# Performance work log

Hardware: AMD Instinct MI355X
Metric: run time of the kernel (lower is better)

The kernel has to match this reference:

```python
import jax, jax.numpy as jnp
import numpy as np

H = 16  # attention heads


def setup_inputs() -> dict:
    key = jax.random.key(0)
    k0, k1, k2 = jax.random.split(key, 3)
    B, T, C = 2, 2048, 1024
    x = jax.random.normal(k0, (B, T, C), dtype=jnp.float32)
    W_attn = jax.random.normal(k1, (3 * C, C), dtype=jnp.float32) * 0.02
    W_proj = jax.random.normal(k2, (C, C), dtype=jnp.float32) * 0.02
    b_proj = jnp.zeros((C,), dtype=jnp.float32)
    return {"x": x, "W_attn": W_attn, "W_proj": W_proj, "b_proj": b_proj}


def reference(x, W_attn, W_proj, b_proj):
    # Eval-mode (dropout = identity), rotational_embeddings=False, flash=False path.
    B, T, C = x.shape
    d = C // H
    qkv = jnp.einsum('btc,fc->btf', x, W_attn)          # [B,T,3C] fused QKV proj
    q, k, v = jnp.split(qkv, 3, axis=-1)
    # [B,T,C] -> [B,H,T,d]
    q = q.reshape(B, T, H, d).transpose(0, 2, 1, 3)
    k = k.reshape(B, T, H, d).transpose(0, 2, 1, 3)
    v = v.reshape(B, T, H, d).transpose(0, 2, 1, 3)
    scale = 1.0 / np.sqrt(d).astype(np.float32)
    att = jnp.einsum('bhqd,bhkd->bhqk', q, k) * scale    # full TxT scores (no mask)
    att = jax.nn.softmax(att, axis=-1)
    y = jnp.einsum('bhqk,bhkd->bhqd', att, v)            # [B,H,T,d]
    y = y.transpose(0, 2, 1, 3).reshape(B, T, C)
    return jnp.einsum('btc,oc->bto', y, W_proj) + b_proj
```

## Files before the change

### kernel.cpp

```cpp
#include <hip/hip_runtime.h>
#include <hip/hip_bf16.h>
#include <stdint.h>

typedef __attribute__((ext_vector_type(8))) short bf16x8;
typedef __attribute__((ext_vector_type(4))) float f32x4;
typedef __attribute__((ext_vector_type(4))) unsigned u32x4;

#define MFMA16(A,B,C) __builtin_amdgcn_mfma_f32_16x16x32_bf16(A,B,C,0,0,0)


__device__ inline void gld_lds16(const __hip_bfloat16* g, __hip_bfloat16* l) {
  __builtin_amdgcn_global_load_lds(
      (const __attribute__((address_space(1))) void*)g,
      (__attribute__((address_space(3))) void*)l, 16, 0, 0);
}

__device__ inline unsigned pkbf(float a, float b) {
  __hip_bfloat162 t = __float22bfloat162_rn(float2{a, b});
  return *(unsigned*)&t;
}

__device__ inline void quad_mix(unsigned &a, unsigned &b) {
#if __has_builtin(__builtin_amdgcn_permlane32_swap) && __has_builtin(__builtin_amdgcn_permlane16_swap)
  auto r1 = __builtin_amdgcn_permlane32_swap(a, b, false, false);
  auto r2 = __builtin_amdgcn_permlane16_swap(r1[0], r1[1], false, false);
  a = r2[0];
  b = r2[1];
#else
  int lane = (int)(threadIdx.x & 63);
  int g = lane >> 4;
  int lm = lane & 15;
  int slo = (((g << 1) & 3) << 4) | lm;
  int shi = ((((g << 1) | 1) & 3) << 4) | lm;
  unsigned t0 = (unsigned)__shfl((int)a, slo, 64);
  unsigned t1 = (unsigned)__shfl((int)b, slo, 64);
  unsigned t2 = (unsigned)__shfl((int)a, shi, 64);
  unsigned t3 = (unsigned)__shfl((int)b, shi, 64);
  bool hi = g >= 2;
  unsigned na = hi ? t1 : t0;
  unsigned nb = hi ? t3 : t2;
  a = na;
  b = nb;
#endif
}

__global__ __launch_bounds__(256)
void cvt_bf16(const float* __restrict__ s0, __hip_bfloat16* __restrict__ d0, int n0,
              const float* __restrict__ s1, __hip_bfloat16* __restrict__ d1, int n1,
              const float* __restrict__ s2, __hip_bfloat16* __restrict__ d2, int n2)
{
  const float* s; __hip_bfloat16* d; int n;
  if      (blockIdx.y == 0) { s = s0; d = d0; n = n0; }
  else if (blockIdx.y == 1) { s = s1; d = d1; n = n1; }
  else                      { s = s2; d = d2; n = n2; }
  int idx = (blockIdx.x * 256 + threadIdx.x) * 8;
  if (idx >= n) return;
  float4 u0 = *(const float4*)(s + idx);
  float4 u1 = *(const float4*)(s + idx + 4);
  __hip_bfloat16 t[8];
  t[0] = __float2bfloat16(u0.x); t[1] = __float2bfloat16(u0.y);
  t[2] = __float2bfloat16(u0.z); t[3] = __float2bfloat16(u0.w);
  t[4] = __float2bfloat16(u1.x); t[5] = __float2bfloat16(u1.y);
  t[6] = __float2bfloat16(u1.z); t[7] = __float2bfloat16(u1.w);
  *(int4*)(d + idx) = *(const int4*)t;
}

template<int BM, int BN, typename TC>
__global__ __launch_bounds__(256)
void gemm_bt(const __hip_bfloat16* __restrict__ A,
             const __hip_bfloat16* __restrict__ B,
             TC* __restrict__ C,
             const float* __restrict__ bias,
             __hip_bfloat16* __restrict__ vtg,
             int M, int N, int K)
{
  constexpr int MI = BM / 32;
  constexpr int NJ = BN / 32;
  constexpr int NP = (BM + BN) / 64;

  __shared__ __align__(16) __hip_bfloat16 As[BM * 32];
  __shared__ __align__(16) __hip_bfloat16 Bs[BN * 32];

  const int tid  = threadIdx.x;
  const int lane = tid & 63;
  const int w    = tid >> 6;
  const int lm   = lane & 15;
  const int g    = lane >> 4;

  const int bm = blockIdx.y * BM;
  const int bn = blockIdx.x * BN;
  const int rm = (w >> 1) * (BM / 2);
  const int cn = (w & 1) * (BN / 2);

  const f32x4 fzero = {0.0f, 0.0f, 0.0f, 0.0f};
  f32x4 acc[MI][NJ];
  for (int i = 0; i < MI; i++)
    for (int j = 0; j < NJ; j++)
      acc[i][j] = fzero;

  for (int k0 = 0; k0 < K; k0 += 32) {
    __syncthreads();
#pragma unroll
    for (int p = 0; p < NP; p++) {
      int c = tid + p * 256;
      if (c < BM * 4)
        gld_lds16(&A[(size_t)(bm + (c >> 2)) * K + k0 + (c & 3) * 8], &As[c * 8]);
      else {
        int cb = c - BM * 4;
        gld_lds16(&B[(size_t)(bn + (cb >> 2)) * K + k0 + (cb & 3) * 8], &Bs[cb * 8]);
      }
    }
    __syncthreads();

    bf16x8 af[MI], bfr[NJ];
#pragma unroll
    for (int i = 0; i < MI; i++)
      af[i] = *(const bf16x8*)&As[(rm + 16 * i + lm) * 32 + 8 * g];
#pragma unroll
    for (int j = 0; j < NJ; j++)
      bfr[j] = *(const bf16x8*)&Bs[(cn + 16 * j + lm) * 32 + 8 * g];
#pragma unroll
    for (int i = 0; i < MI; i++)
#pragma unroll
      for (int j = 0; j < NJ; j++)
        acc[i][j] = MFMA16(af[i], bfr[j], acc[i][j]);
  }

  if (vtg != nullptr && bn >= 2048) {
#pragma unroll
    for (int j = 0; j < NJ; j++) {
      int colv = bn + cn + 16 * j + lm - 2048;
      int vh = colv >> 6, dd = colv & 63;
#pragma unroll
      for (int i = 0; i < MI; i++) {
        int m0 = bm + rm + 16 * i + 4 * g;
        int bb = m0 >> 11, t0 = m0 & 2047;
        __hip_bfloat16 t4[4];
#pragma unroll
        for (int r = 0; r < 4; r++) t4[r] = __float2bfloat16(acc[i][j][r]);
        *(int2*)&vtg[((size_t)(bb * 16 + vh) * 64 + dd) * 2048 + t0] =
            *(const int2*)t4;
      }
    }
    return;
  }

  const float qs = (vtg != nullptr && bn < 1024) ? (0.125f * 1.4426950408889634f)
                                                 : 1.0f;
#pragma unroll
  for (int j = 0; j < NJ; j++) {
    int coln = bn + cn + 16 * j + lm;
    float bv = bias ? bias[coln] : 0.0f;
#pragma unroll
    for (int i = 0; i < MI; i++) {
#pragma unroll
      for (int r = 0; r < 4; r++) {
        int rowm = bm + rm + 16 * i + 4 * g + r;
        float v = acc[i][j][r] * qs + bv;
        if constexpr (sizeof(TC) == 2)
          C[(size_t)rowm * N + coln] = __float2bfloat16(v);
        else
          C[(size_t)rowm * N + coln] = v;
      }
    }
  }
}

__global__ __launch_bounds__(256)
void mha(const __hip_bfloat16* __restrict__ qkv,
         const __hip_bfloat16* __restrict__ vtg,
         __hip_bfloat16* __restrict__ yout,
         __hip_bfloat16* __restrict__ po,
         float* __restrict__ pl,
         int nsteps)
{
  const int T = 2048, F = 3072, Cc = 1024;
  const int bh = blockIdx.x;
  const int b  = bh >> 4, h = bh & 15;
  const int qb0 = blockIdx.y * 128;
  const int z   = blockIdx.z;
  const int kvb = z * 32 * nsteps;

  const int tid  = threadIdx.x;
  const int lane = tid & 63;
  const int w    = tid >> 6;
  const int lm   = lane & 15;
  const int g    = lane >> 4;

  __shared__ __align__(16) __hip_bfloat16 Ks[2][32 * 64];
  __shared__ __align__(16) __hip_bfloat16 Vs[2][64 * 32];

  const size_t rowbase = (size_t)b * T * F;
  const int hoff = h * 64;
  const __hip_bfloat16* Kbase = qkv + rowbase + 1024 + hoff;
  const __hip_bfloat16* Vtb   = vtg + (size_t)(b * 16 + h) * 64 * 2048;

  const int qw = qb0 + 32 * w;
  bf16x8 aq[2][2];
#pragma unroll
  for (int mt = 0; mt < 2; mt++)
#pragma unroll
    for (int e = 0; e < 2; e++)
      aq[mt][e] = *(const bf16x8*)
          &qkv[rowbase + (size_t)(qw + 16 * mt + lm) * F + hoff + 32 * e + 8 * g];

  const f32x4 fzero = {0.0f, 0.0f, 0.0f, 0.0f};
  const short one_bf = (short)0x3f80;
  const bf16x8 vone = {one_bf, one_bf, one_bf, one_bf,
                       one_bf, one_bf, one_bf, one_bf};
  f32x4 yacc[2][4];
  f32x4 yl[2];
#pragma unroll
  for (int mt = 0; mt < 2; mt++) {
    yl[mt] = fzero;
#pragma unroll
    for (int c = 0; c < 4; c++) yacc[mt][c] = fzero;
  }

  const int r0  = tid >> 3;
  const int swK = (tid & 7) ^ (r0 & 7);
  const int vdd = tid >> 2;
  const int vk  = (tid & 3) ^ ((tid >> 3) & 3);
  const int sxK = lm & 7;
  const int sxV = (lm >> 1) & 3;

  gld_lds16(Kbase + (size_t)(kvb + r0) * F + swK * 8, &Ks[0][tid * 8]);
  gld_lds16(Vtb + (size_t)vdd * 2048 + kvb + vk * 8, &Vs[0][tid * 8]);

  for (int t = 0; t < nsteps; t++) {
    const int buf = t & 1;
    __syncthreads();
    if (t + 1 < nsteps) {
      const int kvn = kvb + (t + 1) * 32;
      gld_lds16(Kbase + (size_t)(kvn + r0) * F + swK * 8, &Ks[buf ^ 1][tid * 8]);
      gld_lds16(Vtb + (size_t)vdd * 2048 + kvn + vk * 8, &Vs[buf ^ 1][tid * 8]);
    }

    bf16x8 kf[2][2];
#pragma unroll
    for (int c2 = 0; c2 < 2; c2++) {
      kf[c2][0] = *(const bf16x8*)&Ks[buf][(16 * c2 + lm) * 64 + ((0 + g) ^ sxK) * 8];
      kf[c2][1] = *(const bf16x8*)&Ks[buf][(16 * c2 + lm) * 64 + ((4 + g) ^ sxK) * 8];
    }

    bf16x8 ap[2];
#pragma unroll
    for (int mt = 0; mt < 2; mt++) {
      f32x4 st[2];
      __builtin_amdgcn_s_setprio(1);
#pragma unroll
      for (int c2 = 0; c2 < 2; c2++) {
        st[c2] = MFMA16(kf[c2][0], aq[mt][0], fzero);
        st[c2] = MFMA16(kf[c2][1], aq[mt][1], st[c2]);
      }
      __builtin_amdgcn_s_setprio(0);

      unsigned pkv[2][2];
#pragma unroll
      for (int c2 = 0; c2 < 2; c2++)
#pragma unroll
        for (int u = 0; u < 2; u++) {
          float p0 = __builtin_amdgcn_exp2f(st[c2][2 * u]);
          float p1 = __builtin_amdgcn_exp2f(st[c2][2 * u + 1]);
          pkv[c2][u] = pkbf(p0, p1);
        }

      unsigned f0 = pkv[0][0], f2 = pkv[1][0];
      quad_mix(f0, f2);
      unsigned f1 = pkv[0][1], f3 = pkv[1][1];
      quad_mix(f1, f3);
      u32x4 fv = {f0, f1, f2, f3};
      ap[mt] = __builtin_bit_cast(bf16x8, fv);
    }

    __builtin_amdgcn_s_setprio(1);
#pragma unroll
    for (int c = 0; c < 4; c++) {
      bf16x8 bv = *(const bf16x8*)&Vs[buf][(16 * c + lm) * 32 + (g ^ sxV) * 8];
      yacc[0][c] = MFMA16(ap[0], bv, yacc[0][c]);
      yacc[1][c] = MFMA16(ap[1], bv, yacc[1][c]);
    }
    yl[0] = MFMA16(ap[0], vone, yl[0]);
    yl[1] = MFMA16(ap[1], vone, yl[1]);
    __builtin_amdgcn_s_setprio(0);
  }

#pragma unroll
  for (int mt = 0; mt < 2; mt++) {
    if (yout != nullptr) {
      float rv[4];
#pragma unroll
      for (int r = 0; r < 4; r++)
        rv[r] = 1.0f / yl[mt][r];
#pragma unroll
      for (int c = 0; c < 4; c++)
#pragma unroll
        for (int r = 0; r < 4; r++) {
          int qrow = qw + 16 * mt + 4 * g + r;
          yout[(size_t)(b * T + qrow) * Cc + hoff + 16 * c + lm] =
              __float2bfloat16(yacc[mt][c][r] * rv[r]);
        }
    } else {
      __hip_bfloat16* pz = po + (size_t)z * 4096 * 1024;
      float* plz = pl + (size_t)z * 4096 * 16;
#pragma unroll
      for (int c = 0; c < 4; c++)
#pragma unroll
        for (int r = 0; r < 4; r++) {
          int qrow = qw + 16 * mt + 4 * g + r;
          pz[(size_t)(b * T + qrow) * Cc + hoff + 16 * c + lm] =
              __float2bfloat16(yacc[mt][c][r]);
        }
      if (lm == 0) {
#pragma unroll
        for (int r = 0; r < 4; r++)
          plz[(b * T + qw + 16 * mt + 4 * g + r) * 16 + h] = yl[mt][r];
      }
    }
  }
}

template<int Z>
__global__ __launch_bounds__(256)
void combine(const __hip_bfloat16* __restrict__ po,
             const float* __restrict__ pl,
             __hip_bfloat16* __restrict__ y)
{
  int idx = (blockIdx.x * 256 + threadIdx.x) * 8;
  int row = idx >> 10, c = idx & 1023, h = c >> 6;
  float l = 0.0f;
#pragma unroll
  for (int zi = 0; zi < Z; zi++)
    l += pl[zi * 4096 * 16 + row * 16 + h];
  float rinv = 1.0f / l;
  float acc[8] = {0.f, 0.f, 0.f, 0.f, 0.f, 0.f, 0.f, 0.f};
#pragma unroll
  for (int zi = 0; zi < Z; zi++) {
    int4 raw = *(const int4*)(po + (size_t)zi * 4096 * 1024 + idx);
    const __hip_bfloat16* pa = (const __hip_bfloat16*)&raw;
#pragma unroll
    for (int j = 0; j < 8; j++) acc[j] += __bfloat162float(pa[j]);
  }
  __hip_bfloat16 t[8];
#pragma unroll
  for (int j = 0; j < 8; j++) t[j] = __float2bfloat16(acc[j] * rinv);
  *(int4*)(y + idx) = *(const int4*)t;
}

extern "C" void kernel_launch(void* const* d_in, const int* in_sizes, int n_in,
                              void* d_out, int out_size, void* d_ws, size_t ws_size,
                              hipStream_t stream)
{
  const float* x  = (const float*)d_in[0];
  const float* Wa = (const float*)d_in[1];
  const float* Wp = (const float*)d_in[2];
  const float* bp = (const float*)d_in[3];
  float* out = (float*)d_out;

  const int BT = 4096, C = 1024, F3 = 3072;
  char* ws = (char*)d_ws;
  __hip_bfloat16* qkv  = (__hip_bfloat16*)ws;
  __hip_bfloat16* vtg  = (__hip_bfloat16*)(ws + 25165824);
  __hip_bfloat16* xbf  = (__hip_bfloat16*)(ws + 33554432);
  __hip_bfloat16* yb   = xbf;
  __hip_bfloat16* Wabf = (__hip_bfloat16*)(ws + 41943040);
  __hip_bfloat16* Wpbf = (__hip_bfloat16*)(ws + 48234496);
  __hip_bfloat16* Opar = (__hip_bfloat16*)(ws + 50331648);
  float*          lpar = (float*)(ws + 67108864);
  const size_t need_split = 67633152;

  cvt_bf16<<<dim3(2048, 3), 256, 0, stream>>>(
      x, xbf, BT * C, Wa, Wabf, F3 * C, Wp, Wpbf, C * C);
  gemm_bt<128, 128, __hip_bfloat16>
      <<<dim3(F3 / 128, BT / 128), 256, 0, stream>>>(xbf, Wabf, qkv, nullptr, vtg,
                                                     BT, F3, C);
  if (ws_size >= need_split) {
    mha<<<dim3(32, 16, 2), 256, 0, stream>>>(qkv, vtg, nullptr, Opar, lpar, 32);
    combine<2><<<dim3(BT * C / 2048), 256, 0, stream>>>(Opar, lpar, yb);
  } else {
    mha<<<dim3(32, 16, 1), 256, 0, stream>>>(qkv, vtg, yb, nullptr, nullptr, 64);
  }
  gemm_bt<64, 128, float>
      <<<dim3(C / 128, BT / 64), 256, 0, stream>>>(yb, Wpbf, out, bp, nullptr,
                                                   BT, C, C);
}
```

Measured before the change: 207.0 us.

## Triple-buffer K/V LDS staging with explicit vmcnt waits in attention loop

Changes the attention kernel's K/V shared-memory staging from double to triple buffering, prefetching two tiles ahead. A manual s_waitcnt vmcnt plus a raw s_barrier replace __syncthreads, so loads for the following tile can stay in flight across the barrier. The intent is to hide more global-load latency per step. In exchange it uses 50% more LDS, which may reduce occupancy, and the hand-written waitcnt logic is fragile if the compiler issues other vector-memory ops.

After: 206.5 us. No clear change (-0.2%).

```diff
diff --git a/kernel.cpp b/kernel.cpp
--- a/kernel.cpp
+++ b/kernel.cpp
@@ -187,8 +187,8 @@
   const int lm   = lane & 15;
   const int g    = lane >> 4;
 
-  __shared__ __align__(16) __hip_bfloat16 Ks[2][32 * 64];
-  __shared__ __align__(16) __hip_bfloat16 Vs[2][64 * 32];
+  __shared__ __align__(16) __hip_bfloat16 Ks[3][32 * 64];
+  __shared__ __align__(16) __hip_bfloat16 Vs[3][64 * 32];
 
   const size_t rowbase = (size_t)b * T * F;
   const int hoff = h * 64;
@@ -224,23 +224,38 @@
   const int sxK = lm & 7;
   const int sxV = (lm >> 1) & 3;
 
-  gld_lds16(Kbase + (size_t)(kvb + r0) * F + swK * 8, &Ks[0][tid * 8]);
-  gld_lds16(Vtb + (size_t)vdd * 2048 + kvb + vk * 8, &Vs[0][tid * 8]);
-
+  auto stage = [&](int tt, int bb) {
+    const int kvn = kvb + tt * 32;
+    gld_lds16(Kbase + (size_t)(kvn + r0) * F + swK * 8, &Ks[bb][tid * 8]);
+    gld_lds16(Vtb + (size_t)vdd * 2048 + kvn + vk * 8, &Vs[bb][tid * 8]);
+  };
+
+  stage(0, 0);
+  if (nsteps > 1) stage(1, 1);
+
+  int bcur = 0;
   for (int t = 0; t < nsteps; t++) {
-    const int buf = t & 1;
-    __syncthreads();
-    if (t + 1 < nsteps) {
-      const int kvn = kvb + (t + 1) * 32;
-      gld_lds16(Kbase + (size_t)(kvn + r0) * F + swK * 8, &Ks[buf ^ 1][tid * 8]);
-      gld_lds16(Vtb + (size_t)vdd * 2048 + kvn + vk * 8, &Vs[buf ^ 1][tid * 8]);
-    }
+    if (t + 1 < nsteps)
+      asm volatile("s_waitcnt vmcnt(2)" ::: "memory");
+    else
+      asm volatile("s_waitcnt vmcnt(0)" ::: "memory");
+    __builtin_amdgcn_s_barrier();
+    __builtin_amdgcn_sched_barrier(0);
+
+    if (t + 2 < nsteps) {
+      int bnx = bcur + 2; if (bnx >= 3) bnx -= 3;
+      stage(t + 2, bnx);
+    }
+    __builtin_amdgcn_sched_barrier(0);
+
+    const __hip_bfloat16* Kb = Ks[bcur];
+    const __hip_bfloat16* Vb = Vs[bcur];
 
     bf16x8 kf[2][2];
 #pragma unroll
     for (int c2 = 0; c2 < 2; c2++) {
-      kf[c2][0] = *(const bf16x8*)&Ks[buf][(16 * c2 + lm) * 64 + ((0 + g) ^ sxK) * 8];
-      kf[c2][1] = *(const bf16x8*)&Ks[buf][(16 * c2 + lm) * 64 + ((4 + g) ^ sxK) * 8];
+      kf[c2][0] = *(const bf16x8*)&Kb[(16 * c2 + lm) * 64 + ((0 + g) ^ sxK) * 8];
+      kf[c2][1] = *(const bf16x8*)&Kb[(16 * c2 + lm) * 64 + ((4 + g) ^ sxK) * 8];
     }
 
     bf16x8 ap[2];
@@ -276,13 +291,15 @@
     __builtin_amdgcn_s_setprio(1);
 #pragma unroll
     for (int c = 0; c < 4; c++) {
-      bf16x8 bv = *(const bf16x8*)&Vs[buf][(16 * c + lm) * 32 + (g ^ sxV) * 8];
+      bf16x8 bv = *(const bf16x8*)&Vb[(16 * c + lm) * 32 + (g ^ sxV) * 8];
       yacc[0][c] = MFMA16(ap[0], bv, yacc[0][c]);
       yacc[1][c] = MFMA16(ap[1], bv, yacc[1][c]);
     }
     yl[0] = MFMA16(ap[0], vone, yl[0]);
     yl[1] = MFMA16(ap[1], vone, yl[1]);
     __builtin_amdgcn_s_setprio(0);
+
+    bcur = bcur + 1; if (bcur >= 3) bcur = 0;
   }
 
 #pragma unroll
```

## Double attention KV tile to 64 keys and swap grid axes for query blocks

Applied to the files above, without the earlier changes.

The attention kernel now processes 64 keys per step instead of 32, which halves the number of loop iterations and barriers. K and V tiles use a unified XOR swizzle, and each thread issues two async global-to-LDS loads per tile. The grid is reordered so query blocks run along x and batch-head along y, which changes block scheduling order and possibly L2 reuse of K/V. It costs more LDS and more live registers for the score tiles, which may reduce occupancy.

Measured after the change: 207.7 us. About the same (+0.3%).

```diff
diff --git a/kernel.cpp b/kernel.cpp
--- a/kernel.cpp
+++ b/kernel.cpp
@@ -175,11 +175,11 @@
          int nsteps)
 {
   const int T = 2048, F = 3072, Cc = 1024;
-  const int bh = blockIdx.x;
+  const int bh = blockIdx.y;
   const int b  = bh >> 4, h = bh & 15;
-  const int qb0 = blockIdx.y * 128;
+  const int qb0 = blockIdx.x * 128;
   const int z   = blockIdx.z;
-  const int kvb = z * 32 * nsteps;
+  const int kvb = z * 64 * nsteps;
 
   const int tid  = threadIdx.x;
   const int lane = tid & 63;
@@ -187,8 +187,8 @@
   const int lm   = lane & 15;
   const int g    = lane >> 4;
 
-  __shared__ __align__(16) __hip_bfloat16 Ks[2][32 * 64];
-  __shared__ __align__(16) __hip_bfloat16 Vs[2][64 * 32];
+  __shared__ __align__(16) __hip_bfloat16 Ks[2][64 * 64];
+  __shared__ __align__(16) __hip_bfloat16 Vs[2][64 * 64];
 
   const size_t rowbase = (size_t)b * T * F;
   const int hoff = h * 64;
@@ -217,71 +217,88 @@
     for (int c = 0; c < 4; c++) yacc[mt][c] = fzero;
   }
 
-  const int r0  = tid >> 3;
-  const int swK = (tid & 7) ^ (r0 & 7);
-  const int vdd = tid >> 2;
-  const int vk  = (tid & 3) ^ ((tid >> 3) & 3);
-  const int sxK = lm & 7;
-  const int sxV = (lm >> 1) & 3;
-
-  gld_lds16(Kbase + (size_t)(kvb + r0) * F + swK * 8, &Ks[0][tid * 8]);
-  gld_lds16(Vtb + (size_t)vdd * 2048 + kvb + vk * 8, &Vs[0][tid * 8]);
+  const int sx = lm & 7;
+
+  auto stage = [&](int tt, int bb) {
+    const int kvn = kvb + tt * 64;
+#pragma unroll
+    for (int p = 0; p < 2; p++) {
+      int c = tid + p * 256;
+      int row = c >> 3, sl = c & 7, gc = sl ^ (row & 7);
+      gld_lds16(Kbase + (size_t)(kvn + row) * F + gc * 8, &Ks[bb][c * 8]);
+    }
+#pragma unroll
+    for (int p = 0; p < 2; p++) {
+      int c = tid + p * 256;
+      int row = c >> 3, sl = c & 7, gc = sl ^ (row & 7);
+      gld_lds16(Vtb + (size_t)row * 2048 + kvn + gc * 8, &Vs[bb][c * 8]);
+    }
+  };
+
+  stage(0, 0);
 
   for (int t = 0; t < nsteps; t++) {
     const int buf = t & 1;
     __syncthreads();
-    if (t + 1 < nsteps) {
-      const int kvn = kvb + (t + 1) * 32;
-      gld_lds16(Kbase + (size_t)(kvn + r0) * F + swK * 8, &Ks[buf ^ 1][tid * 8]);
-      gld_lds16(Vtb + (size_t)vdd * 2048 + kvn + vk * 8, &Vs[buf ^ 1][tid * 8]);
-    }
-
-    bf16x8 kf[2][2];
-#pragma unroll
-    for (int c2 = 0; c2 < 2; c2++) {
-      kf[c2][0] = *(const bf16x8*)&Ks[buf][(16 * c2 + lm) * 64 + ((0 + g) ^ sxK) * 8];
-      kf[c2][1] = *(const bf16x8*)&Ks[buf][(16 * c2 + lm) * 64 + ((4 + g) ^ sxK) * 8];
-    }
-
-    bf16x8 ap[2];
+    if (t + 1 < nsteps) stage(t + 1, buf ^ 1);
+
+    const __hip_bfloat16* Kb = Ks[buf];
+    const __hip_bfloat16* Vb = Vs[buf];
+
+    f32x4 st[2][4];
+    __builtin_amdgcn_s_setprio(1);
+#pragma unroll
+    for (int c2 = 0; c2 < 4; c2++) {
+      bf16x8 k0 = *(const bf16x8*)&Kb[(16 * c2 + lm) * 64 + ((0 + g) ^ sx) * 8];
+      bf16x8 k1 = *(const bf16x8*)&Kb[(16 * c2 + lm) * 64 + ((4 + g) ^ sx) * 8];
+      st[0][c2] = MFMA16(k0, aq[0][0], fzero);
+      st[0][c2] = MFMA16(k1, aq[0][1], st[0][c2]);
+      st[1][c2] = MFMA16(k0, aq[1][0], fzero);
+      st[1][c2] = MFMA16(k1, aq[1][1], st[1][c2]);
+    }
+    __builtin_amdgcn_s_setprio(0);
+
+    bf16x8 ap[2][2];
 #pragma unroll
     for (int mt = 0; mt < 2; mt++) {
-      f32x4 st[2];
-      __builtin_amdgcn_s_setprio(1);
-#pragma unroll
-      for (int c2 = 0; c2 < 2; c2++) {
-        st[c2] = MFMA16(kf[c2][0], aq[mt][0], fzero);
-        st[c2] = MFMA16(kf[c2][1], aq[mt][1], st[c2]);
-      }
-      __builtin_amdgcn_s_setprio(0);
-
-      unsigned pkv[2][2];
-#pragma unroll
-      for (int c2 = 0; c2 < 2; c2++)
-#pragma unroll
-        for (int u = 0; u < 2; u++) {
-          float p0 = __builtin_amdgcn_exp2f(st[c2][2 * u]);
-          float p1 = __builtin_amdgcn_exp2f(st[c2][2 * u + 1]);
-          pkv[c2][u] = pkbf(p0, p1);
+#pragma unroll
+      for (int hf = 0; hf < 2; hf++) {
+        unsigned pkv[2][2];
+#pragma unroll
+        for (int cc = 0; cc < 2; cc++) {
+          const f32x4 &s4 = st[mt][2 * hf + cc];
+#pragma unroll
+          for (int u = 0; u < 2; u++) {
+            float p0 = __builtin_amdgcn_exp2f(s4[2 * u]);
+            float p1 = __builtin_amdgcn_exp2f(s4[2 * u + 1]);
+            pkv[cc][u] = pkbf(p0, p1);
+          }
         }
-
-      unsigned f0 = pkv[0][0], f2 = pkv[1][0];
-      quad_mix(f0, f2);
-      unsigned f1 = pkv[0][1], f3 = pkv[1][1];
-      quad_mix(f1, f3);
-      u32x4 fv = {f0, f1, f2, f3};
-      ap[mt] = __builtin_bit_cast(bf16x8, fv);
+        unsigned f0 = pkv[0][0], f2 = pkv[1][0];
+        quad_mix(f0, f2);
+        unsigned f1 = pkv[0][1], f3 = pkv[1][1];
+        quad_mix(f1, f3);
+        u32x4 fv = {f0, f1, f2, f3};
+        ap[mt][hf] = __builtin_bit_cast(bf16x8, fv);
+      }
     }
 
     __builtin_amdgcn_s_setprio(1);
 #pragma unroll
     for (int c = 0; c < 4; c++) {
-      bf16x8 bv = *(const bf16x8*)&Vs[buf][(16 * c + lm) * 32 + (g ^ sxV) * 8];
-      yacc[0][c] = MFMA16(ap[0], bv, yacc[0][c]);
-      yacc[1][c] = MFMA16(ap[1], bv, yacc[1][c]);
-    }
-    yl[0] = MFMA16(ap[0], vone, yl[0]);
-    yl[1] = MFMA16(ap[1], vone, yl[1]);
+#pragma unroll
+      for (int hf = 0; hf < 2; hf++) {
+        bf16x8 bv = *(const bf16x8*)
+            &Vb[(16 * c + lm) * 64 + (((hf << 2) | g) ^ sx) * 8];
+        yacc[0][c] = MFMA16(ap[0][hf], bv, yacc[0][c]);
+        yacc[1][c] = MFMA16(ap[1][hf], bv, yacc[1][c]);
+      }
+    }
+#pragma unroll
+    for (int mt = 0; mt < 2; mt++) {
+      yl[mt] = MFMA16(ap[mt][0], vone, yl[mt]);
+      yl[mt] = MFMA16(ap[mt][1], vone, yl[mt]);
+    }
     __builtin_amdgcn_s_setprio(0);
   }
 
@@ -375,10 +392,10 @@
       <<<dim3(F3 / 128, BT / 128), 256, 0, stream>>>(xbf, Wabf, qkv, nullptr, vtg,
                                                      BT, F3, C);
   if (ws_size >= need_split) {
-    mha<<<dim3(32, 16, 2), 256, 0, stream>>>(qkv, vtg, nullptr, Opar, lpar, 32);
+    mha<<<dim3(16, 32, 2), 256, 0, stream>>>(qkv, vtg, nullptr, Opar, lpar, 16);
     combine<2><<<dim3(BT * C / 2048), 256, 0, stream>>>(Opar, lpar, yb);
   } else {
-    mha<<<dim3(32, 16, 1), 256, 0, stream>>>(qkv, vtg, yb, nullptr, nullptr, 64);
+    mha<<<dim3(16, 32, 1), 256, 0, stream>>>(qkv, vtg, yb, nullptr, nullptr, 32);
   }
   gemm_bt<64, 128, float>
       <<<dim3(C / 128, BT / 64), 256, 0, stream>>>(yb, Wpbf, out, bp, nullptr,
```
